# Performance work log

Hardware: AMD Instinct MI355X
Metric: run time of the kernel (lower is better)

The kernel has to match this reference:

```python
import jax, jax.numpy as jnp
import numpy as np

EMB = 2048
N_HEADS = 16
HEAD_DIM = 128
N_KV = 4
ROPE_BASE = 10000.0
B, S = 2, 2048


def _rope(x, cos, sin):
    # x: [B,S,h,d]; cos/sin: [1,S,1,d//2]
    x1, x2 = x[..., ::2], x[..., 1::2]
    return jnp.concatenate([x1 * cos - x2 * sin, x1 * sin + x2 * cos], axis=-1)


def setup_inputs() -> dict:
    key = jax.random.key(0)
    ks = jax.random.split(key, 5)
    x = jax.random.normal(ks[0], (B, S, EMB), dtype=jnp.float32)
    wq = jax.random.normal(ks[1], (EMB, N_HEADS * HEAD_DIM), dtype=jnp.float32) * 0.02
    wk = jax.random.normal(ks[2], (EMB, N_KV * HEAD_DIM), dtype=jnp.float32) * 0.02
    wv = jax.random.normal(ks[3], (EMB, N_KV * HEAD_DIM), dtype=jnp.float32) * 0.02
    wo = jax.random.normal(ks[4], (N_HEADS * HEAD_DIM, EMB), dtype=jnp.float32) * 0.02
    mask = jnp.tril(jnp.ones((S, S), dtype=bool))[None, None]  # [1,1,S,S] causal
    return {"x": x, "wq": wq, "wk": wk, "wv": wv, "wo": wo, "mask": mask}


def reference(x, wq, wk, wv, wo, mask):
    b, s, _ = x.shape
    q = (x @ wq).reshape(b, s, N_HEADS, HEAD_DIM)
    k = (x @ wk).reshape(b, s, N_KV, HEAD_DIM)
    v = (x @ wv).reshape(b, s, N_KV, HEAD_DIM)

    pos = jnp.arange(s, dtype=jnp.float32)
    dim_range = jnp.arange(0, HEAD_DIM, 2, dtype=jnp.float32)
    freqs = 1.0 / ROPE_BASE ** (dim_range / HEAD_DIM)
    angles = pos[:, None] * freqs[None, :]            # [S, d/2]
    cos = jnp.cos(angles)[None, :, None, :]           # [1,S,1,d/2]
    sin = jnp.sin(angles)[None, :, None, :]

    q = _rope(q, cos, sin)
    k = _rope(k, cos, sin)

    rep = N_HEADS // N_KV
    k = jnp.tile(k, (1, 1, rep, 1))  # matches torch .repeat on group dim
    v = jnp.tile(v, (1, 1, rep, 1))

    scale = 1.0 / jnp.sqrt(jnp.float32(HEAD_DIM))
    scores = jnp.einsum('bqhd,bkhd->bhqk', q, k) * scale  # [B,H,S,S]
    scores = jnp.where(mask, scores, -jnp.inf)
    attn = jax.nn.softmax(scores, axis=-1)  # dropout is identity in eval
    out = jnp.einsum('bhqk,bkhd->bqhd', attn, v).reshape(b, s, N_HEADS * HEAD_DIM)
    return out @ wo
```

## Files before the change

kernel.cpp:

```cpp
#include <hip/hip_runtime.h>

#define EMB 2048
#define NH 16
#define NKV 4
#define HD 128
#define SLEN 2048
#define BSZ 2
#define MROWS (BSZ * SLEN)

#define QOFF (BSZ * NH * SLEN * HD)
#define KOFF (BSZ * NKV * SLEN * HD)

typedef __attribute__((ext_vector_type(8))) short bf16x8;
typedef __attribute__((ext_vector_type(4))) float f32x4;
typedef __attribute__((ext_vector_type(2))) float f32x2;
typedef __attribute__((ext_vector_type(4))) short s16x4;

__device__ __forceinline__ short f2bf(float f) {
  union { float f; unsigned u; } v; v.f = f;
  unsigned r = (v.u + 0x7fffu + ((v.u >> 16) & 1u)) >> 16;
  return (short)r;
}

__global__ void rope_tab_k(f32x2* __restrict__ tab) {
  int i = blockIdx.x * blockDim.x + threadIdx.x;
  if (i >= SLEN * 64) return;
  int s = i >> 6, j = i & 63;
  float freq = exp2f(-(float)j * (13.287712379549449f / 64.0f));
  float ang = (float)s * freq;
  float sv, cv;
  sincosf(ang, &sv, &cv);
  f32x2 cs; cs[0] = cv; cs[1] = sv;
  tab[i] = cs;
}

__global__ void cast_bf16_k(const float* __restrict__ in, short* __restrict__ outp, int n) {
  int i = (blockIdx.x * blockDim.x + threadIdx.x) * 4;
  if (i >= n) return;
  f32x4 v = *(const f32x4*)(in + i);
  s16x4 r;
#pragma unroll
  for (int k = 0; k < 4; ++k) r[k] = f2bf(v[k]);
  *(s16x4*)(outp + i) = r;
}

__global__ void transpose_cast_k(const float* __restrict__ in, short* __restrict__ outp,
                                 int R, int C) {
  __shared__ float t[32][33];
  int c0 = blockIdx.x * 32, r0 = blockIdx.y * 32;
  int tx = threadIdx.x, ty = threadIdx.y;
#pragma unroll
  for (int i = 0; i < 4; ++i)
    t[ty + i * 8][tx] = in[(size_t)(r0 + ty + i * 8) * C + (c0 + tx)];
  __syncthreads();
#pragma unroll
  for (int i = 0; i < 4; ++i)
    outp[(size_t)(c0 + ty + i * 8) * R + (r0 + tx)] = f2bf(t[tx][ty + i * 8]);
}

#define GLL16(g, l)                                                        \
  __builtin_amdgcn_global_load_lds(                                        \
      (const __attribute__((address_space(1))) void*)(g),                  \
      (__attribute__((address_space(3))) void*)(l), 16, 0, 0)

template <int EPI>
__global__ __launch_bounds__(256, 2) void gemm_bt_k(
    const short* __restrict__ A, const short* __restrict__ Bt,
    float* __restrict__ Cf, short* __restrict__ Cb,
    int M, int N, int K, const f32x2* __restrict__ rope) {
  __shared__ short lA[3][128 * 32];
  __shared__ short lB[3][128 * 32];
  int tid = threadIdx.x;
  int lane = tid & 63, wid = tid >> 6;
  int m0 = blockIdx.y * 128, n0 = blockIdx.x * 128;
  int wr = (wid >> 1) * 64, wc = (wid & 1) * 64;
  int l16 = lane & 15, lk4 = lane >> 4;
  const int K2B = K * 2;
  const char* Ab = (const char*)A;
  const char* Bb = (const char*)Bt;
  (void)M;

  auto stage = [&](int slot, int k0) {
#pragma unroll
    for (int r = 0; r < 2; ++r) {
      int X = tid * 16 + r * 4096;
      int row = X >> 6, cb = X & 63;
      int logical = cb ^ ((row & 3) << 4);
      GLL16(Ab + (size_t)(m0 + row) * K2B + k0 * 2 + logical, (char*)&lA[slot][0] + X);
      GLL16(Bb + (size_t)(n0 + row) * K2B + k0 * 2 + logical, (char*)&lB[slot][0] + X);
    }
  };
  auto ldA = [&](int slot, int m) {
    int row = wr + m * 16 + l16;
    return *(const bf16x8*)((char*)&lA[slot][0] + row * 64 + ((lk4 * 16) ^ ((row & 3) << 4)));
  };
  auto ldB = [&](int slot, int n) {
    int row = wc + n * 16 + l16;
    return *(const bf16x8*)((char*)&lB[slot][0] + row * 64 + ((lk4 * 16) ^ ((row & 3) << 4)));
  };

  f32x4 acc[4][4] = {};
  stage(0, 0);
  stage(1, 32);
  int nk = K / 32;
  for (int t = 0; t < nk; ++t) {
    int slot = t % 3;
    if (t + 1 < nk) asm volatile("s_waitcnt vmcnt(4)" ::: "memory");
    else            asm volatile("s_waitcnt vmcnt(0)" ::: "memory");
    __builtin_amdgcn_s_barrier();
    __builtin_amdgcn_sched_barrier(0);
    bf16x8 af[4], bfv[4];
#pragma unroll
    for (int m = 0; m < 4; ++m) af[m] = ldA(slot, m);
#pragma unroll
    for (int n = 0; n < 4; ++n) bfv[n] = ldB(slot, n);
    __builtin_amdgcn_s_setprio(1);
#pragma unroll
    for (int m = 0; m < 4; ++m)
#pragma unroll
      for (int n = 0; n < 4; ++n)
        acc[m][n] = __builtin_amdgcn_mfma_f32_16x16x32_bf16(af[m], bfv[n], acc[m][n], 0, 0, 0);
    __builtin_amdgcn_s_setprio(0);
    if (t + 2 < nk) stage((t + 2) % 3, (t + 2) * 32);
  }

  const float SCL2E = 0.08838834764831845f * 1.4426950408889634f;
#pragma unroll
  for (int m = 0; m < 4; ++m) {
#pragma unroll
    for (int n = 0; n < 4; ++n) {
#pragma unroll
      for (int j = 0; j < 4; ++j) {
        int gm = m0 + wr + m * 16 + lk4 * 4 + j;
        int gc = n0 + wc + n * 16 + l16;
        float v = acc[m][n][j];
        if constexpr (EPI == 0) {
          Cf[(size_t)gm * N + gc] = v;
        } else {
          int pos = gm & (SLEN - 1), bb = gm >> 11;
          if (gc < 2560) {
            float p = __shfl_xor(v, 1);
            bool isq = gc < 2048;
            int gcc = isq ? gc : gc - 2048;
            int head = gcc >> 7, d = gcc & 127;
            f32x2 cs = rope[pos * 64 + (d >> 1)];
            float ov = ((d & 1) == 0) ? (v * cs[0] - p * cs[1])
                                      : (p * cs[1] + v * cs[0]);
            if (isq) ov *= SCL2E;
            size_t idx = isq
                ? (((size_t)(bb * NH + head) * SLEN + pos) * HD + d)
                : ((size_t)QOFF + ((size_t)(bb * NKV + head) * SLEN + pos) * HD + d);
            Cb[idx] = f2bf(ov);
          } else {
            int gcc = gc - 2560;
            int head = gcc >> 7, d = gcc & 127;
            Cb[(size_t)QOFF + KOFF + ((size_t)(bb * NKV + head) * HD + d) * SLEN + pos] = f2bf(v);
          }
        }
      }
    }
  }
}

__global__ __launch_bounds__(512, 2) void flash_k(
    const short* __restrict__ Qb, const short* __restrict__ Kb,
    const short* __restrict__ Vt, short* __restrict__ O) {
  __shared__ short lK[4][64 * 128];
  __shared__ short lV[4][128 * 64];
  __shared__ short Plds[8][16][64];

  int tid = threadIdx.x, lane = tid & 63, wid = tid >> 6;
  int bh = blockIdx.y;
  int b = bh >> 4, h = bh & 15, kv = h & 3;
  int l16 = lane & 15, lk4 = lane >> 4;
  int qtA = 15 - (int)blockIdx.x;
  int qtB = (int)blockIdx.x;
  int ntA = 2 * (qtA + 1);
  int ntot = ntA + 2 * (qtB + 1);

  const short* qptr = Qb + (size_t)(b * NH + h) * SLEN * HD;
  const char* kg = (const char*)(Kb + (size_t)(b * NKV + kv) * SLEN * HD);
  const char* vg = (const char*)(Vt + (size_t)(b * NKV + kv) * HD * SLEN);

  int qbw = qtA * 128 + wid * 16;
  bf16x8 aq[4];
#pragma unroll
  for (int c = 0; c < 4; ++c)
    aq[c] = *(const bf16x8*)(qptr + (size_t)(qbw + l16) * HD + c * 32 + lk4 * 8);

  f32x4 o[8] = {};
  float m = -__builtin_inff();
  float lsum = 0.0f;

  char* myP = (char*)&Plds[wid][0][0];
  int swz = (l16 & 7) << 4;
  int swzk = l16 << 4;

  auto stageKV = [&](int buf, int k0) {
#pragma unroll
    for (int r = 0; r < 2; ++r) {
      int X = tid * 16 + r * 8192;
      int row = X >> 8, cb = X & 255;
      GLL16(kg + (size_t)(k0 + row) * 256 + (cb ^ ((row & 15) << 4)),
            (char*)&lK[buf][0] + X);
    }
#pragma unroll
    for (int r = 0; r < 2; ++r) {
      int X = tid * 16 + r * 8192;
      int row = X >> 7, cb = X & 127;
      GLL16(vg + (size_t)row * (SLEN * 2) + k0 * 2 + (cb ^ ((row & 7) << 4)),
            (char*)&lV[buf][0] + X);
    }
  };
  auto k0_of = [&](int t) { return (t < ntA ? t : t - ntA) * 64; };

  auto finalize = [&]() {
    float ls = lsum;
    ls += __shfl_xor(ls, 16);
    ls += __shfl_xor(ls, 32);
    float inv = 1.0f / ls;
    size_t ro = ((size_t)(b * SLEN + qbw + l16)) * (NH * HD) + h * HD;
#pragma unroll
    for (int dt = 0; dt < 8; ++dt) {
      s16x4 r;
#pragma unroll
      for (int j = 0; j < 4; ++j) r[j] = f2bf(o[dt][j] * inv);
      *(s16x4*)(O + ro + dt * 16 + lk4 * 4) = r;
    }
  };

  stageKV(0, k0_of(0));
  stageKV(1, k0_of(1));
  stageKV(2, k0_of(2));

  for (int tt = 0; tt < ntot; ++tt) {
    int rem = ntot - 1 - tt;
    if (rem >= 2)      asm volatile("s_waitcnt vmcnt(8)" ::: "memory");
    else if (rem == 1) asm volatile("s_waitcnt vmcnt(4)" ::: "memory");
    else               asm volatile("s_waitcnt vmcnt(0)" ::: "memory");
    __builtin_amdgcn_s_barrier();
    __builtin_amdgcn_sched_barrier(0);

    if (tt == ntA) {
      finalize();
#pragma unroll
      for (int dt = 0; dt < 8; ++dt) o[dt] = (f32x4){0.f, 0.f, 0.f, 0.f};
      m = -__builtin_inff();
      lsum = 0.0f;
      qbw = qtB * 128 + wid * 16;
#pragma unroll
      for (int c = 0; c < 4; ++c)
        aq[c] = *(const bf16x8*)(qptr + (size_t)(qbw + l16) * HD + c * 32 + lk4 * 8);
    }

    int k0 = k0_of(tt);
    int buf = tt & 3;
    if (k0 < qbw + 16) {
      const char* Kbase = (const char*)&lK[buf][0];
      const char* Vbase = (const char*)&lV[buf][0];
      f32x4 s[4] = {};
      __builtin_amdgcn_s_setprio(1);
#pragma unroll
      for (int c = 0; c < 4; ++c) {
#pragma unroll
        for (int t = 0; t < 4; ++t) {
          bf16x8 bk = *(const bf16x8*)(Kbase + (t * 16 + l16) * 256 + ((c * 64 + lk4 * 16) ^ swzk));
          s[t] = __builtin_amdgcn_mfma_f32_16x16x32_bf16(bk, aq[c], s[t], 0, 0, 0);
        }
      }
      __builtin_amdgcn_s_setprio(0);
      float x[16];
#pragma unroll
      for (int t = 0; t < 4; ++t)
#pragma unroll
        for (int j = 0; j < 4; ++j) x[t * 4 + j] = s[t][j];
      if (k0 + 63 > qbw) {
        int kq = k0 + lk4 * 4 - qbw - l16;
#pragma unroll
        for (int t = 0; t < 4; ++t)
#pragma unroll
          for (int j = 0; j < 4; ++j)
            if (kq + t * 16 + j > 0) x[t * 4 + j] = -3.0e38f;
      }
      float a0 = fmaxf(x[0], x[1]), a1 = fmaxf(x[2], x[3]);
      float a2 = fmaxf(x[4], x[5]), a3 = fmaxf(x[6], x[7]);
      float a4 = fmaxf(x[8], x[9]), a5 = fmaxf(x[10], x[11]);
      float a6 = fmaxf(x[12], x[13]), a7 = fmaxf(x[14], x[15]);
      float b0 = fmaxf(fmaxf(a0, a1), fmaxf(a2, a3));
      float b1 = fmaxf(fmaxf(a4, a5), fmaxf(a6, a7));
      float tm = fmaxf(b0, b1);
      tm = fmaxf(tm, __shfl_xor(tm, 16));
      tm = fmaxf(tm, __shfl_xor(tm, 32));
      float mn = fmaxf(m, tm);
      if (!__all(tm <= m + 8.0f)) {
        float f = __builtin_amdgcn_exp2f(m - mn);
        m = mn;
        lsum *= f;
#pragma unroll
        for (int dt = 0; dt < 8; ++dt) o[dt] *= f;
      }
      float psum = 0.0f;
#pragma unroll
      for (int t = 0; t < 4; ++t) {
        float p0 = __builtin_amdgcn_exp2f(x[t * 4 + 0] - m);
        float p1 = __builtin_amdgcn_exp2f(x[t * 4 + 1] - m);
        float p2 = __builtin_amdgcn_exp2f(x[t * 4 + 2] - m);
        float p3 = __builtin_amdgcn_exp2f(x[t * 4 + 3] - m);
        psum += (p0 + p1) + (p2 + p3);
        unsigned lo, hi;
        asm("v_cvt_pk_bf16_f32 %0, %1, %2" : "=v"(lo) : "v"(p0), "v"(p1));
        asm("v_cvt_pk_bf16_f32 %0, %1, %2" : "=v"(hi) : "v"(p2), "v"(p3));
        unsigned long long dw = ((unsigned long long)hi << 32) | lo;
        *(unsigned long long*)(myP + ((l16 * 128 + t * 32 + lk4 * 8) ^ swz)) = dw;
      }
      lsum += psum;
      asm volatile("s_waitcnt lgkmcnt(0)" ::: "memory");
      __builtin_amdgcn_sched_barrier(0);
      __builtin_amdgcn_s_setprio(1);
#pragma unroll
      for (int hh = 0; hh < 2; ++hh) {
        bf16x8 pa = *(const bf16x8*)(myP + ((l16 * 128 + hh * 64 + lk4 * 16) ^ swz));
#pragma unroll
        for (int dt = 0; dt < 8; ++dt) {
          bf16x8 bv = *(const bf16x8*)(Vbase + (dt * 16 + l16) * 128 + ((hh * 64 + lk4 * 16) ^ swz));
          o[dt] = __builtin_amdgcn_mfma_f32_16x16x32_bf16(bv, pa, o[dt], 0, 0, 0);
        }
      }
      __builtin_amdgcn_s_setprio(0);
    }
    if (tt + 3 < ntot) stageKV((tt + 3) & 3, k0_of(tt + 3));
  }
  finalize();
}

extern "C" void kernel_launch(void* const* d_in, const int* in_sizes, int n_in,
                              void* d_out, int out_size, void* d_ws, size_t ws_size,
                              hipStream_t stream) {
  const float* x  = (const float*)d_in[0];
  const float* wq = (const float*)d_in[1];
  const float* wk = (const float*)d_in[2];
  const float* wv = (const float*)d_in[3];
  const float* wo = (const float*)d_in[4];
  float* out = (float*)d_out;
  char* ws = (char*)d_ws;
  (void)in_sizes; (void)n_in; (void)out_size; (void)ws_size;

  const size_t MB = 1024 * 1024;
  f32x2* rope   = (f32x2*)(ws);
  short* xb     = (short*)(ws + 1 * MB);
  short* wqkvT  = (short*)(ws + 17 * MB);
  short* woT    = (short*)(ws + 29 * MB);
  short* QKVb   = (short*)(ws + 37 * MB);
  short* O      = xb;

  short* Qb = QKVb;
  short* Kb = QKVb + QOFF;
  short* Vt = QKVb + QOFF + KOFF;

  rope_tab_k<<<(SLEN * 64 + 255) / 256, 256, 0, stream>>>(rope);
  cast_bf16_k<<<(MROWS * EMB / 4 + 255) / 256, 256, 0, stream>>>(x, xb, MROWS * EMB);

  dim3 tb(32, 8);
  transpose_cast_k<<<dim3(2048 / 32, 2048 / 32), tb, 0, stream>>>(wq, wqkvT, 2048, 2048);
  transpose_cast_k<<<dim3(512 / 32, 2048 / 32), tb, 0, stream>>>(wk, wqkvT + 2048 * 2048, 2048, 512);
  transpose_cast_k<<<dim3(512 / 32, 2048 / 32), tb, 0, stream>>>(wv, wqkvT + 2560 * 2048, 2048, 512);
  transpose_cast_k<<<dim3(2048 / 32, 2048 / 32), tb, 0, stream>>>(wo, woT, 2048, 2048);

  gemm_bt_k<5><<<dim3(3072 / 128, MROWS / 128), 256, 0, stream>>>(xb, wqkvT, nullptr, QKVb, MROWS, 3072, 2048, rope);

  flash_k<<<dim3(8, BSZ * NH), 512, 0, stream>>>(Qb, Kb, Vt, O);

  gemm_bt_k<0><<<dim3(2048 / 128, MROWS / 128), 256, 0, stream>>>(O, woT, out, nullptr, MROWS, 2048, 2048, rope);
}
```

Before: 211.2 us.

## Fuse prep kernels, swap GEMM grid order, and issue prefetch before MFMAs

Merges the rope table, input cast and four weight transpose-cast launches into one prep kernel that dispatches on block index, cutting launch count and inter-kernel gaps. Swaps the GEMM grid axes so consecutive blocks walk M instead of N, which changes which tiles share L2. Moves the next-stage global-to-LDS prefetch ahead of the MFMA block so loads overlap compute. The prefetch now targets the slot read in the previous iteration, so it depends on the barrier at the top of each iteration to avoid overwriting data still being read.

```diff
diff --git a/kernel.cpp b/kernel.cpp
--- a/kernel.cpp
+++ b/kernel.cpp
@@ -22,40 +22,55 @@
   return (short)r;
 }
 
-__global__ void rope_tab_k(f32x2* __restrict__ tab) {
-  int i = blockIdx.x * blockDim.x + threadIdx.x;
-  if (i >= SLEN * 64) return;
-  int s = i >> 6, j = i & 63;
-  float freq = exp2f(-(float)j * (13.287712379549449f / 64.0f));
-  float ang = (float)s * freq;
-  float sv, cv;
-  sincosf(ang, &sv, &cv);
-  f32x2 cs; cs[0] = cv; cs[1] = sv;
-  tab[i] = cs;
-}
-
-__global__ void cast_bf16_k(const float* __restrict__ in, short* __restrict__ outp, int n) {
-  int i = (blockIdx.x * blockDim.x + threadIdx.x) * 4;
-  if (i >= n) return;
-  f32x4 v = *(const f32x4*)(in + i);
-  s16x4 r;
-#pragma unroll
-  for (int k = 0; k < 4; ++k) r[k] = f2bf(v[k]);
-  *(s16x4*)(outp + i) = r;
-}
-
-__global__ void transpose_cast_k(const float* __restrict__ in, short* __restrict__ outp,
-                                 int R, int C) {
+#define PB0 8192
+#define PB1 (PB0 + 512)
+#define PB2 (PB1 + 4096)
+#define PB3 (PB2 + 1024)
+#define PB4 (PB3 + 1024)
+#define PB5 (PB4 + 4096)
+
+__global__ __launch_bounds__(256) void prep_k(
+    const float* __restrict__ x, const float* __restrict__ wq,
+    const float* __restrict__ wk, const float* __restrict__ wv,
+    const float* __restrict__ wo, f32x2* __restrict__ rope,
+    short* __restrict__ xb, short* __restrict__ wqkvT, short* __restrict__ woT) {
+  int bid = blockIdx.x, tid = threadIdx.x;
+  if (bid < PB0) {
+    int i = (bid * 256 + tid) * 4;
+    f32x4 v = *(const f32x4*)(x + i);
+    s16x4 r;
+#pragma unroll
+    for (int k = 0; k < 4; ++k) r[k] = f2bf(v[k]);
+    *(s16x4*)(xb + i) = r;
+    return;
+  }
+  if (bid < PB1) {
+    int i = (bid - PB0) * 256 + tid;
+    int s = i >> 6, j = i & 63;
+    float freq = exp2f(-(float)j * (13.287712379549449f / 64.0f));
+    float ang = (float)s * freq;
+    float sv, cv;
+    sincosf(ang, &sv, &cv);
+    f32x2 cs; cs[0] = cv; cs[1] = sv;
+    rope[i] = cs;
+    return;
+  }
+  const float* src; int C, local; short* dst;
+  if (bid < PB2)      { src = wq; C = 2048; local = bid - PB1; dst = wqkvT; }
+  else if (bid < PB3) { src = wk; C = 512;  local = bid - PB2; dst = wqkvT + 2048 * 2048; }
+  else if (bid < PB4) { src = wv; C = 512;  local = bid - PB3; dst = wqkvT + 2560 * 2048; }
+  else                { src = wo; C = 2048; local = bid - PB4; dst = woT; }
   __shared__ float t[32][33];
-  int c0 = blockIdx.x * 32, r0 = blockIdx.y * 32;
-  int tx = threadIdx.x, ty = threadIdx.y;
+  int nbx = C >> 5;
+  int c0 = (local % nbx) * 32, r0 = (local / nbx) * 32;
+  int tx = tid & 31, ty = tid >> 5;
 #pragma unroll
   for (int i = 0; i < 4; ++i)
-    t[ty + i * 8][tx] = in[(size_t)(r0 + ty + i * 8) * C + (c0 + tx)];
+    t[ty + i * 8][tx] = src[(size_t)(r0 + ty + i * 8) * C + (c0 + tx)];
   __syncthreads();
 #pragma unroll
   for (int i = 0; i < 4; ++i)
-    outp[(size_t)(c0 + ty + i * 8) * R + (r0 + tx)] = f2bf(t[tx][ty + i * 8]);
+    dst[(size_t)(c0 + ty + i * 8) * 2048 + (r0 + tx)] = f2bf(t[tx][ty + i * 8]);
 }
 
 #define GLL16(g, l)                                                        \
@@ -72,7 +87,7 @@
   __shared__ short lB[3][128 * 32];
   int tid = threadIdx.x;
   int lane = tid & 63, wid = tid >> 6;
-  int m0 = blockIdx.y * 128, n0 = blockIdx.x * 128;
+  int m0 = blockIdx.x * 128, n0 = blockIdx.y * 128;
   int wr = (wid >> 1) * 64, wc = (wid & 1) * 64;
   int l16 = lane & 15, lk4 = lane >> 4;
   const int K2B = K * 2;
@@ -114,6 +129,7 @@
     for (int m = 0; m < 4; ++m) af[m] = ldA(slot, m);
 #pragma unroll
     for (int n = 0; n < 4; ++n) bfv[n] = ldB(slot, n);
+    if (t + 2 < nk) stage(slot == 2 ? 1 : (slot == 1 ? 0 : 2), (t + 2) * 32);
     __builtin_amdgcn_s_setprio(1);
 #pragma unroll
     for (int m = 0; m < 4; ++m)
@@ -121,7 +137,6 @@
       for (int n = 0; n < 4; ++n)
         acc[m][n] = __builtin_amdgcn_mfma_f32_16x16x32_bf16(af[m], bfv[n], acc[m][n], 0, 0, 0);
     __builtin_amdgcn_s_setprio(0);
-    if (t + 2 < nk) stage((t + 2) % 3, (t + 2) * 32);
   }
 
   const float SCL2E = 0.08838834764831845f * 1.4426950408889634f;
@@ -357,18 +372,11 @@
   short* Kb = QKVb + QOFF;
   short* Vt = QKVb + QOFF + KOFF;
 
-  rope_tab_k<<<(SLEN * 64 + 255) / 256, 256, 0, stream>>>(rope);
-  cast_bf16_k<<<(MROWS * EMB / 4 + 255) / 256, 256, 0, stream>>>(x, xb, MROWS * EMB);
-
-  dim3 tb(32, 8);
-  transpose_cast_k<<<dim3(2048 / 32, 2048 / 32), tb, 0, stream>>>(wq, wqkvT, 2048, 2048);
-  transpose_cast_k<<<dim3(512 / 32, 2048 / 32), tb, 0, stream>>>(wk, wqkvT + 2048 * 2048, 2048, 512);
-  transpose_cast_k<<<dim3(512 / 32, 2048 / 32), tb, 0, stream>>>(wv, wqkvT + 2560 * 2048, 2048, 512);
-  transpose_cast_k<<<dim3(2048 / 32, 2048 / 32), tb, 0, stream>>>(wo, woT, 2048, 2048);
-
-  gemm_bt_k<5><<<dim3(3072 / 128, MROWS / 128), 256, 0, stream>>>(xb, wqkvT, nullptr, QKVb, MROWS, 3072, 2048, rope);
+  prep_k<<<PB5, 256, 0, stream>>>(x, wq, wk, wv, wo, rope, xb, wqkvT, woT);
+
+  gemm_bt_k<5><<<dim3(MROWS / 128, 3072 / 128), 256, 0, stream>>>(xb, wqkvT, nullptr, QKVb, MROWS, 3072, 2048, rope);
 
   flash_k<<<dim3(8, BSZ * NH), 512, 0, stream>>>(Qb, Kb, Vt, O);
 
-  gemm_bt_k<0><<<dim3(2048 / 128, MROWS / 128), 256, 0, stream>>>(O, woT, out, nullptr, MROWS, 2048, 2048, rope);
-}
+  gemm_bt_k<0><<<dim3(MROWS / 128, 2048 / 128), 256, 0, stream>>>(O, woT, out, nullptr, MROWS, 2048, 2048, rope);
+}
```

Result: faster. 188.2 us (-10.9%).
